# Kernel optimization log

Hardware: AMD Instinct MI355X
Metric: run time of the kernel (lower is better)

The kernel has to match this reference:

```python
import jax, jax.numpy as jnp
import numpy as np

N_AGENTS = 16
NE = 128
ED = 96          # entity_shape (entity_last_action=False)
HE = 128         # hypernet_embed
MD = 32          # mixing_embed_dim
NH = 4           # attn heads
HD = HE // NH
BS, T = 32, 50


def setup_inputs() -> dict:
    key = jax.random.key(0)
    ks = jax.random.split(key, 20)
    def lin(k, i, o):
        return (jax.random.normal(k, (i, o), jnp.float32) / np.sqrt(i)).astype(jnp.float32)
    inp = {
        "agent_qs": jax.random.normal(ks[0], (BS, T, N_AGENTS), jnp.float32),
        "entities": jax.random.normal(ks[1], (BS, T, NE, ED), jnp.float32),
        "entity_mask": jax.random.uniform(ks[2], (BS, T, NE)) < 0.15,  # True = masked/inactive
    }
    for i, p in enumerate(["w1", "v"]):
        b = 3 + i * 6
        inp[p + "_fc1_w"] = lin(ks[b], ED, HE)
        inp[p + "_fc1_b"] = jnp.zeros((HE,), jnp.float32)
        inp[p + "_attn_in_w"] = lin(ks[b + 1], HE, 3 * HE)   # in_trans (no bias)
        inp[p + "_attn_out_w"] = lin(ks[b + 2], HE, HE)
        inp[p + "_attn_out_b"] = jnp.zeros((HE,), jnp.float32)
        inp[p + "_fc2_w"] = lin(ks[b + 3], HE, MD)
        inp[p + "_fc2_b"] = jnp.zeros((MD,), jnp.float32)
    return inp


def _hypernet(x, emask, fc1_w, fc1_b, in_w, out_w, out_b, fc2_w, fc2_b, mode):
    # x: [B, ne, ed], emask: [B, ne] bool (True = masked)
    B = x.shape[0]
    x1 = jax.nn.relu(x @ fc1_w + fc1_b)                         # [B, ne, HE]
    agent_mask = emask[:, :N_AGENTS]                            # [B, na]
    af = agent_mask.astype(x.dtype)
    ef = emask.astype(x.dtype)
    # attn_mask = 1 - (1-agent)(1-entity); 1 => masked pair
    pre = (1.0 - (1.0 - af)[:, :, None] * (1.0 - ef)[:, None, :]) > 0.5  # [B, na, ne]
    qkv = x1 @ in_w                                             # [B, ne, 3*HE]
    q, k, v = jnp.split(qkv, 3, axis=-1)
    q = q[:, :N_AGENTS].reshape(B, N_AGENTS, NH, HD)
    k = k.reshape(B, NE, NH, HD)
    v = v.reshape(B, NE, NH, HD)
    logits = jnp.einsum('bqhd,bkhd->bhqk', q, k) / np.float32(np.sqrt(HD))
    logits = jnp.where(pre[:, None], jnp.float32(-1e9), logits)
    w = jax.nn.softmax(logits, axis=-1)                         # [B, NH, na, ne]
    # rows where every entity is masked: torch softmax gives NaN -> filled with 0
    all_masked = jnp.all(pre, axis=-1)                          # [B, na]
    w = jnp.where(all_masked[:, None, :, None], 0.0, w)
    attn = jnp.einsum('bhqk,bkhd->bqhd', w, v).reshape(B, N_AGENTS, HE)
    out = attn @ out_w + out_b
    out = jnp.where(agent_mask[:, :, None], 0.0, out)           # post_mask fill
    x3 = out @ fc2_w + fc2_b
    x3 = jnp.where(agent_mask[:, :, None], 0.0, x3)             # [B, na, MD]
    if mode == 'alt_vector':
        return x3.mean(axis=2)                                  # [B, na]
    return x3.mean(axis=(1, 2))                                 # [B]  (scalar mode)


def reference(agent_qs, entities, entity_mask,
              w1_fc1_w, w1_fc1_b, w1_attn_in_w, w1_attn_out_w, w1_attn_out_b, w1_fc2_w, w1_fc2_b,
              v_fc1_w, v_fc1_b, v_attn_in_w, v_attn_out_w, v_attn_out_b, v_fc2_w, v_fc2_b):
    bs, max_t, ne, ed = entities.shape
    ents = entities.reshape(bs * max_t, ne, ed)
    emask = entity_mask.reshape(bs * max_t, ne)
    qs = agent_qs.reshape(-1, N_AGENTS)
    w1 = _hypernet(ents, emask, w1_fc1_w, w1_fc1_b, w1_attn_in_w, w1_attn_out_w,
                   w1_attn_out_b, w1_fc2_w, w1_fc2_b, 'alt_vector')   # [B, na]
    w1 = jnp.abs(w1)                                            # softmax_mixing_weights=False
    v = _hypernet(ents, emask, v_fc1_w, v_fc1_b, v_attn_in_w, v_attn_out_w,
                  v_attn_out_b, v_fc2_w, v_fc2_b, 'scalar')     # [B]
    q_tot = (qs * w1).sum(axis=1) + v
    return q_tot.reshape(bs, max_t, 1)
```

## Files before the change

kernel.cpp:

```cpp
#include <hip/hip_runtime.h>
#include <hip/hip_bf16.h>


#define NA 16
#define NEn 128
#define EDm 96
#define ST 136

typedef __attribute__((ext_vector_type(8))) short bf16x8;
typedef __attribute__((ext_vector_type(4))) float f32x4;

#define MFMA(a, b, c) __builtin_amdgcn_mfma_f32_16x16x32_bf16((a), (b), (c), 0, 0, 0)
#define LGKM0() __asm__ volatile("s_waitcnt lgkmcnt(0)" ::: "memory")

#define OFF_W1 0
#define OFF_WQ 12288
#define OFF_WK 28672
#define OFF_WV 45056
#define OFF_WO 61440
#define OFF_W2 77824
#define HYPE 81920
#define WS_FLAG_OFF 327680

__device__ __forceinline__ unsigned short f2bf(float f) {
  unsigned u = __float_as_uint(f);
  u += 0x7fffu + ((u >> 16) & 1u);
  return (unsigned short)(u >> 16);
}

__device__ __forceinline__ unsigned cvt_pk2(float lo, float hi) {
  union { __hip_bfloat162 h2; unsigned u; } cv;
  cv.h2 = __float22bfloat162_rn(float2{lo, hi});
  return cv.u;
}

__device__ __forceinline__ void ctile_store(unsigned short* dst, int row0,
                                            int col, f32x4 v) {
  unsigned x = cvt_pk2(v[0], v[1]);
  unsigned y = cvt_pk2(v[2], v[3]);
  unsigned ox = (unsigned)__shfl_xor((int)x, 1);
  unsigned oy = (unsigned)__shfl_xor((int)y, 1);
  unsigned w0, w1;
  int ra;
  if ((threadIdx.x & 1) == 0) {
    ra = 0;
    w0 = (x & 0xffffu) | (ox << 16);
    w1 = (x >> 16) | (ox & 0xffff0000u);
  } else {
    ra = 2;
    w0 = (oy & 0xffffu) | (y << 16);
    w1 = (oy >> 16) | (y & 0xffff0000u);
  }
  *(unsigned*)(dst + (row0 + ra) * ST + (col & ~1)) = w0;
  *(unsigned*)(dst + (row0 + ra + 1) * ST + (col & ~1)) = w1;
}

__global__ void prep_kernel(const float* __restrict__ w_fc1w,
                            const float* __restrict__ w_inw,
                            const float* __restrict__ w_outw,
                            const float* __restrict__ w_fc2w,
                            const float* __restrict__ v_fc1w,
                            const float* __restrict__ v_inw,
                            const float* __restrict__ v_outw,
                            const float* __restrict__ v_fc2w,
                            const unsigned char* __restrict__ mask,
                            unsigned short* __restrict__ ws,
                            int* __restrict__ flag) {
  if (blockIdx.x == 80) {
    const uint4 v = *(const uint4*)(mask + threadIdx.x * 16);
    const unsigned nz = (v.x | v.y | v.z | v.w) & 0xffffff00u;
    const int any = __syncthreads_or((int)(nz != 0));
    if (threadIdx.x == 0) *flag = (any == 0) ? 1 : 0;
    return;
  }
  const int g = blockIdx.x * 256 + threadIdx.x;
  const int p = (g >= 10240) ? 1 : 0;
  const int i = g - p * 10240;
  const int l = i & 63;
  const int tt = i >> 6;
  const int lhi = l >> 4, lo = l & 15;
  const float* fc1w = p ? v_fc1w : w_fc1w;
  const float* inw = p ? v_inw : w_inw;
  const float* outw = p ? v_outw : w_outw;
  const float* fc2w = p ? v_fc2w : w_fc2w;
  unsigned short* wsp = ws + p * HYPE;

  float v8[8];
  unsigned short* dst;
  if (tt < 24) {
    const int nt = tt / 3, kt = tt - nt * 3;
    const float* src = fc1w + (kt * 32 + lhi * 8) * 128 + nt * 16 + lo;
#pragma unroll
    for (int j = 0; j < 8; ++j) v8[j] = src[j * 128];
    dst = wsp + OFF_W1 + tt * 512 + l * 8;
  } else if (tt < 56) {
    const int t2 = tt - 24;
    const int nt = t2 >> 2, kt = t2 & 3;
    const float* src = inw + (kt * 32 + lhi * 8) * 384 + nt * 16 + lo;
#pragma unroll
    for (int j = 0; j < 8; ++j) v8[j] = src[j * 384] * 0.17677669529663687f;
    dst = wsp + OFF_WQ + t2 * 512 + l * 8;
  } else if (tt < 88) {
    const int t2 = tt - 56;
    const int h = t2 >> 3, nt = t2 & 7;
    const float* src = inw + (nt * 16 + lo) * 384 + 128 + h * 32 + lhi * 8;
#pragma unroll
    for (int j = 0; j < 8; ++j) v8[j] = src[j];
    dst = wsp + OFF_WK + t2 * 512 + l * 8;
  } else if (tt < 120) {
    const int t2 = tt - 88;
    const int kt = t2 & 3, q = t2 >> 2;
    const int h = q >> 1, mt = q & 1;
    const float* src =
        inw + (kt * 32 + lhi * 8) * 384 + 256 + h * 32 + mt * 16 + lo;
#pragma unroll
    for (int j = 0; j < 8; ++j) v8[j] = src[j * 384];
    dst = wsp + OFF_WV + t2 * 512 + l * 8;
  } else if (tt < 152) {
    const int t2 = tt - 120;
    const int nt = t2 >> 2, kt = t2 & 3;
    const float* src = outw + (kt * 32 + lhi * 8) * 128 + nt * 16 + lo;
#pragma unroll
    for (int j = 0; j < 8; ++j) v8[j] = src[j * 128];
    dst = wsp + OFF_WO + t2 * 512 + l * 8;
  } else {
    const int t2 = tt - 152;
    const int nt = t2 >> 2, kt = t2 & 3;
    const float* src = fc2w + (kt * 32 + lhi * 8) * 32 + nt * 16 + lo;
#pragma unroll
    for (int j = 0; j < 8; ++j) v8[j] = src[j * 32];
    dst = wsp + OFF_W2 + t2 * 512 + l * 8;
  }
  bf16x8 o;
#pragma unroll
  for (int j = 0; j < 8; ++j) o[j] = (short)f2bf(v8[j]);
  *(bf16x8*)dst = o;
}

#define SMEM_BYTES 52480

__global__ __launch_bounds__(256, 2) void qmix_mfma(
    const float* __restrict__ agent_qs, const float* __restrict__ entities,
    const unsigned char* __restrict__ emask_g,
    const unsigned short* __restrict__ wsw, const int* __restrict__ mflag,
    const float* __restrict__ w_fc1b, const float* __restrict__ w_outb,
    const float* __restrict__ w_fc2b, const float* __restrict__ v_fc1b,
    const float* __restrict__ v_outb, const float* __restrict__ v_fc2b,
    float* __restrict__ out_g) {
  const int t = threadIdx.x;
  const int wv = t >> 6;
  const int ln = t & 63;
  const int lr = ln & 15;
  const int lq = ln >> 4;
  const int b = blockIdx.x >> 1;
  const int p = blockIdx.x & 1;
  const float* ents = entities + (size_t)b * (NEn * EDm);

  __shared__ __align__(16) unsigned char smem[SMEM_BYTES];
  unsigned short* sx1 = (unsigned short*)smem;
  unsigned short* sSlice = sx1 + 17408;
  unsigned short* sattn = sSlice;
  unsigned short* sout = sSlice + 16 * ST;
  float* sres = (float*)(smem + 52224);
  unsigned char* sm = smem + 52352;
  unsigned short* sS = sSlice + wv * 16 * ST;

  const int is_i32 = *mflag;
  int mv = 1;
  if (t < NEn) {
    if (is_i32)
      mv = (((const int*)emask_g)[(size_t)b * NEn + t] != 0) ? 1 : 0;
    else
      mv = (emask_g[(size_t)b * NEn + t] != 0) ? 1 : 0;
    sm[t] = (unsigned char)mv;
  }
  const int allE = __syncthreads_and(mv);

  const unsigned short* wsb = wsw + (size_t)p * HYPE;
  const float* fc1b = p ? v_fc1b : w_fc1b;
  const float* outb = p ? v_outb : w_outb;
  const float* fc2b = p ? v_fc2b : w_fc2b;

  {
#pragma unroll
    for (int mi = 0; mi < 2; ++mi) {
      const int mt = wv * 2 + mi;
      bf16x8 af[3];
      const float* erow = ents + (mt * 16 + lr) * EDm + lq * 8;
#pragma unroll
      for (int kt = 0; kt < 3; ++kt) {
        float4 u = *(const float4*)(erow + kt * 32);
        float4 w = *(const float4*)(erow + kt * 32 + 4);
        union { unsigned u32[4]; bf16x8 v8; } cv;
        cv.u32[0] = cvt_pk2(u.x, u.y);
        cv.u32[1] = cvt_pk2(u.z, u.w);
        cv.u32[2] = cvt_pk2(w.x, w.y);
        cv.u32[3] = cvt_pk2(w.z, w.w);
        af[kt] = cv.v8;
      }
#pragma unroll
      for (int nt = 0; nt < 8; ++nt) {
        f32x4 acc = {0.f, 0.f, 0.f, 0.f};
        const unsigned short* bp = wsb + OFF_W1 + (nt * 3) * 512 + ln * 8;
#pragma unroll
        for (int kt = 0; kt < 3; ++kt)
          acc = MFMA(af[kt], *(const bf16x8*)(bp + kt * 512), acc);
        const float bias = fc1b[nt * 16 + lr];
        f32x4 r;
        r[0] = fmaxf(acc[0] + bias, 0.f); r[1] = fmaxf(acc[1] + bias, 0.f);
        r[2] = fmaxf(acc[2] + bias, 0.f); r[3] = fmaxf(acc[3] + bias, 0.f);
        ctile_store(sx1, mt * 16 + lq * 4, nt * 16 + lr, r);
      }
    }
  }
  __syncthreads();

  {
    bf16x8 aq[4];
#pragma unroll
    for (int kt = 0; kt < 4; ++kt)
      aq[kt] = *(const bf16x8*)(sx1 + lr * ST + kt * 32 + lq * 8);
#pragma unroll
    for (int ni = 0; ni < 2; ++ni) {
      const int nt = wv * 2 + ni;
      f32x4 acc = {0.f, 0.f, 0.f, 0.f};
      const unsigned short* bp = wsb + OFF_WQ + (nt * 4) * 512 + ln * 8;
#pragma unroll
      for (int kt = 0; kt < 4; ++kt)
        acc = MFMA(aq[kt], *(const bf16x8*)(bp + kt * 512), acc);
      ctile_store(sS, lq * 4, ni * 16 + lr, acc);
    }
  }
  bf16x8 wk[8];
#pragma unroll
  for (int nt = 0; nt < 8; ++nt)
    wk[nt] = *(const bf16x8*)(wsb + OFF_WK + (wv * 8 + nt) * 512 + ln * 8);
  LGKM0();
  const bf16x8 aQ = *(const bf16x8*)(sS + lr * ST + lq * 8);

  {
    f32x4 Cw[8];
#pragma unroll
    for (int nt = 0; nt < 8; ++nt) {
      f32x4 acc = {0.f, 0.f, 0.f, 0.f};
      Cw[nt] = MFMA(aQ, wk[nt], acc);
    }
#pragma unroll
    for (int nt = 0; nt < 8; ++nt)
      ctile_store(sS, lq * 4, nt * 16 + lr, Cw[nt]);
  }
  LGKM0();
  bf16x8 aw[4];
#pragma unroll
  for (int kt = 0; kt < 4; ++kt)
    aw[kt] = *(const bf16x8*)(sS + lr * ST + kt * 32 + lq * 8);

  f32x4 Cl[8];
  __builtin_amdgcn_s_setprio(1);
#pragma unroll
  for (int nt = 0; nt < 8; ++nt) {
    f32x4 acc = {0.f, 0.f, 0.f, 0.f};
#pragma unroll
    for (int kt = 0; kt < 4; ++kt) {
      const bf16x8 bx =
          *(const bf16x8*)(sx1 + (nt * 16 + lr) * ST + kt * 32 + lq * 8);
      acc = MFMA(aw[kt], bx, acc);
    }
    Cl[nt] = acc;
  }
  __builtin_amdgcn_s_setprio(0);

  {
    float lv[8][4];
#pragma unroll
    for (int nt = 0; nt < 8; ++nt) {
      const int eM = sm[nt * 16 + lr];
#pragma unroll
      for (int r = 0; r < 4; ++r) lv[nt][r] = eM ? -1e9f : Cl[nt][r];
    }
    float mx[4], sl[4];
#pragma unroll
    for (int r = 0; r < 4; ++r) {
      float m = lv[0][r];
#pragma unroll
      for (int nt = 1; nt < 8; ++nt) m = fmaxf(m, lv[nt][r]);
      mx[r] = m;
    }
#pragma unroll
    for (int k = 1; k < 16; k <<= 1)
#pragma unroll
      for (int r = 0; r < 4; ++r) mx[r] = fmaxf(mx[r], __shfl_xor(mx[r], k));
    float ex[8][4];
#pragma unroll
    for (int r = 0; r < 4; ++r) sl[r] = 0.f;
#pragma unroll
    for (int nt = 0; nt < 8; ++nt)
#pragma unroll
      for (int r = 0; r < 4; ++r) {
        ex[nt][r] = __expf(lv[nt][r] - mx[r]);
        sl[r] += ex[nt][r];
      }
#pragma unroll
    for (int k = 1; k < 16; k <<= 1)
#pragma unroll
      for (int r = 0; r < 4; ++r) sl[r] += __shfl_xor(sl[r], k);
    float sc[4];
#pragma unroll
    for (int r = 0; r < 4; ++r)
      sc[r] = ((int)sm[lq * 4 + r] | allE) ? 0.f : (1.f / sl[r]);
#pragma unroll
    for (int nt = 0; nt < 8; ++nt) {
      f32x4 wv4;
#pragma unroll
      for (int r = 0; r < 4; ++r) wv4[r] = ex[nt][r] * sc[r];
      ctile_store(sS, lq * 4, nt * 16 + lr, wv4);
    }
  }
  LGKM0();
  bf16x8 aw2[4];
#pragma unroll
  for (int kt = 0; kt < 4; ++kt)
    aw2[kt] = *(const bf16x8*)(sS + lr * ST + kt * 32 + lq * 8);

  f32x4 Cv[2][8];
  __builtin_amdgcn_s_setprio(1);
#pragma unroll
  for (int mt = 0; mt < 2; ++mt) {
    bf16x8 av[4];
#pragma unroll
    for (int kt = 0; kt < 4; ++kt)
      av[kt] = *(const bf16x8*)(wsb + OFF_WV +
                                (((wv * 2 + mt) * 4) + kt) * 512 + ln * 8);
#pragma unroll
    for (int nt = 0; nt < 8; ++nt) {
      f32x4 acc = {0.f, 0.f, 0.f, 0.f};
#pragma unroll
      for (int kt = 0; kt < 4; ++kt) {
        const bf16x8 bx =
            *(const bf16x8*)(sx1 + (nt * 16 + lr) * ST + kt * 32 + lq * 8);
        acc = MFMA(av[kt], bx, acc);
      }
      Cv[mt][nt] = acc;
    }
  }
  __builtin_amdgcn_s_setprio(0);
  __syncthreads();

  {
#pragma unroll
    for (int mt = 0; mt < 2; ++mt)
#pragma unroll
      for (int nt = 0; nt < 8; ++nt)
        ctile_store(sx1, wv * 32 + mt * 16 + lq * 4, nt * 16 + lr,
                    Cv[mt][nt]);
  }
  LGKM0();
  {
#pragma unroll
    for (int ntd = 0; ntd < 2; ++ntd) {
      f32x4 acc = {0.f, 0.f, 0.f, 0.f};
#pragma unroll
      for (int kt = 0; kt < 4; ++kt) {
        const bf16x8 bv = *(const bf16x8*)(sx1 + (wv * 32 + ntd * 16 + lr) *
                                                     ST +
                                           kt * 32 + lq * 8);
        acc = MFMA(aw2[kt], bv, acc);
      }
      ctile_store(sattn, lq * 4, wv * 32 + ntd * 16 + lr, acc);
    }
  }
  bf16x8 wo[2][4];
#pragma unroll
  for (int ni = 0; ni < 2; ++ni) {
    const unsigned short* bp =
        wsb + OFF_WO + ((wv * 2 + ni) * 4) * 512 + ln * 8;
#pragma unroll
    for (int kt = 0; kt < 4; ++kt)
      wo[ni][kt] = *(const bf16x8*)(bp + kt * 512);
  }
  __syncthreads();

  {
    bf16x8 aa[4];
#pragma unroll
    for (int kt = 0; kt < 4; ++kt)
      aa[kt] = *(const bf16x8*)(sattn + lr * ST + kt * 32 + lq * 8);
#pragma unroll
    for (int ni = 0; ni < 2; ++ni) {
      const int nt = wv * 2 + ni;
      f32x4 acc = {0.f, 0.f, 0.f, 0.f};
#pragma unroll
      for (int kt = 0; kt < 4; ++kt)
        acc = MFMA(aa[kt], wo[ni][kt], acc);
      const float bj = outb[nt * 16 + lr];
      f32x4 r;
      r[0] = acc[0] + bj; r[1] = acc[1] + bj;
      r[2] = acc[2] + bj; r[3] = acc[3] + bj;
      ctile_store(sout, lq * 4, nt * 16 + lr, r);
    }
  }
  bf16x8 w2f[2][4];
#pragma unroll
  for (int nt = 0; nt < 2; ++nt) {
    const unsigned short* bp = wsb + OFF_W2 + (nt * 4) * 512 + ln * 8;
#pragma unroll
    for (int kt = 0; kt < 4; ++kt)
      w2f[nt][kt] = *(const bf16x8*)(bp + kt * 512);
  }
  __syncthreads();

  {
    bf16x8 ao[4];
#pragma unroll
    for (int kt = 0; kt < 4; ++kt)
      ao[kt] = *(const bf16x8*)(sout + lr * ST + kt * 32 + lq * 8);
    f32x4 Cx[2];
#pragma unroll
    for (int nt = 0; nt < 2; ++nt) {
      f32x4 acc = {0.f, 0.f, 0.f, 0.f};
#pragma unroll
      for (int kt = 0; kt < 4; ++kt)
        acc = MFMA(ao[kt], w2f[nt][kt], acc);
      Cx[nt] = acc;
    }
    const float b0 = fc2b[lr], b1 = fc2b[16 + lr];
    float rs[4];
#pragma unroll
    for (int r = 0; r < 4; ++r) {
      const int row = lq * 4 + r;
      rs[r] = sm[row] ? 0.f : (Cx[0][r] + b0 + Cx[1][r] + b1);
    }
#pragma unroll
    for (int k = 1; k < 16; k <<= 1)
#pragma unroll
      for (int r = 0; r < 4; ++r) rs[r] += __shfl_xor(rs[r], k);
    if (wv == 0 && lr == 0) {
#pragma unroll
      for (int r = 0; r < 4; ++r) {
        const int q = lq * 4 + r;
        sres[q] = p ? rs[r] : fabsf(rs[r]) * (1.f / 32.f);
      }
    }
  }

  __syncthreads();
  if (t == 0) {
    float s = 0.f;
    if (p == 0) {
      const float* qs = agent_qs + (size_t)b * NA;
#pragma unroll
      for (int q = 0; q < NA; ++q) s += qs[q] * sres[q];
    } else {
#pragma unroll
      for (int q = 0; q < NA; ++q) s += sres[q];
      s *= (1.f / 512.f);
    }
    atomicAdd(out_g + b, s);
  }
}

extern "C" void kernel_launch(void* const* d_in, const int* in_sizes, int n_in,
                              void* d_out, int out_size, void* d_ws,
                              size_t ws_size, hipStream_t stream) {
  (void)n_in; (void)out_size; (void)ws_size;
  const int nb = in_sizes[0] / NA;
  unsigned short* wsw = (unsigned short*)d_ws;
  int* mflag = (int*)((char*)d_ws + WS_FLAG_OFF);

  hipLaunchKernelGGL(prep_kernel, dim3(81), dim3(256), 0, stream,
                     (const float*)d_in[3], (const float*)d_in[5],
                     (const float*)d_in[6], (const float*)d_in[8],
                     (const float*)d_in[10], (const float*)d_in[12],
                     (const float*)d_in[13], (const float*)d_in[15],
                     (const unsigned char*)d_in[2], wsw, mflag);
  hipLaunchKernelGGL(qmix_mfma, dim3(nb * 2), dim3(256), 0, stream,
                     (const float*)d_in[0], (const float*)d_in[1],
                     (const unsigned char*)d_in[2], (const unsigned short*)wsw,
                     (const int*)mflag, (const float*)d_in[4],
                     (const float*)d_in[7], (const float*)d_in[9],
                     (const float*)d_in[11], (const float*)d_in[14],
                     (const float*)d_in[16], (float*)d_out);
}
```

Baseline: 253.0 us.

## Interleave softmax between V-projection halves and hoist entity loads

Splits the V-projection MFMA loop into two halves and places the softmax VALU work between them, so exponentials and shuffles can overlap with matrix-core work. Entity-row global loads are moved to the start of the kernel, before the mask load and block barrier, to hide their latency. The final block barrier is replaced with an LDS wait, since the result row is written and read within wave 0. The cost is more live registers (staged entity values, Cl, Cv0 and the softmax arrays), which may raise VGPR use and lower occupancy.

Result: faster. 243.7 us (-3.7%).

```diff
diff --git a/kernel.cpp b/kernel.cpp
--- a/kernel.cpp
+++ b/kernel.cpp
@@ -165,6 +165,17 @@
   unsigned char* sm = smem + 52352;
   unsigned short* sS = sSlice + wv * 16 * ST;
 
+  float4 eu[2][3], ev[2][3];
+#pragma unroll
+  for (int mi = 0; mi < 2; ++mi) {
+    const float* erow = ents + ((wv * 2 + mi) * 16 + lr) * EDm + lq * 8;
+#pragma unroll
+    for (int kt = 0; kt < 3; ++kt) {
+      eu[mi][kt] = *(const float4*)(erow + kt * 32);
+      ev[mi][kt] = *(const float4*)(erow + kt * 32 + 4);
+    }
+  }
+
   const int is_i32 = *mflag;
   int mv = 1;
   if (t < NEn) {
@@ -186,16 +197,13 @@
     for (int mi = 0; mi < 2; ++mi) {
       const int mt = wv * 2 + mi;
       bf16x8 af[3];
-      const float* erow = ents + (mt * 16 + lr) * EDm + lq * 8;
 #pragma unroll
       for (int kt = 0; kt < 3; ++kt) {
-        float4 u = *(const float4*)(erow + kt * 32);
-        float4 w = *(const float4*)(erow + kt * 32 + 4);
         union { unsigned u32[4]; bf16x8 v8; } cv;
-        cv.u32[0] = cvt_pk2(u.x, u.y);
-        cv.u32[1] = cvt_pk2(u.z, u.w);
-        cv.u32[2] = cvt_pk2(w.x, w.y);
-        cv.u32[3] = cvt_pk2(w.z, w.w);
+        cv.u32[0] = cvt_pk2(eu[mi][kt].x, eu[mi][kt].y);
+        cv.u32[1] = cvt_pk2(eu[mi][kt].z, eu[mi][kt].w);
+        cv.u32[2] = cvt_pk2(ev[mi][kt].x, ev[mi][kt].y);
+        cv.u32[3] = cvt_pk2(ev[mi][kt].z, ev[mi][kt].w);
         af[kt] = cv.v8;
       }
 #pragma unroll
@@ -268,69 +276,14 @@
     }
     Cl[nt] = acc;
   }
-  __builtin_amdgcn_s_setprio(0);
-
-  {
-    float lv[8][4];
-#pragma unroll
-    for (int nt = 0; nt < 8; ++nt) {
-      const int eM = sm[nt * 16 + lr];
-#pragma unroll
-      for (int r = 0; r < 4; ++r) lv[nt][r] = eM ? -1e9f : Cl[nt][r];
-    }
-    float mx[4], sl[4];
-#pragma unroll
-    for (int r = 0; r < 4; ++r) {
-      float m = lv[0][r];
-#pragma unroll
-      for (int nt = 1; nt < 8; ++nt) m = fmaxf(m, lv[nt][r]);
-      mx[r] = m;
-    }
-#pragma unroll
-    for (int k = 1; k < 16; k <<= 1)
-#pragma unroll
-      for (int r = 0; r < 4; ++r) mx[r] = fmaxf(mx[r], __shfl_xor(mx[r], k));
-    float ex[8][4];
-#pragma unroll
-    for (int r = 0; r < 4; ++r) sl[r] = 0.f;
-#pragma unroll
-    for (int nt = 0; nt < 8; ++nt)
-#pragma unroll
-      for (int r = 0; r < 4; ++r) {
-        ex[nt][r] = __expf(lv[nt][r] - mx[r]);
-        sl[r] += ex[nt][r];
-      }
-#pragma unroll
-    for (int k = 1; k < 16; k <<= 1)
-#pragma unroll
-      for (int r = 0; r < 4; ++r) sl[r] += __shfl_xor(sl[r], k);
-    float sc[4];
-#pragma unroll
-    for (int r = 0; r < 4; ++r)
-      sc[r] = ((int)sm[lq * 4 + r] | allE) ? 0.f : (1.f / sl[r]);
-#pragma unroll
-    for (int nt = 0; nt < 8; ++nt) {
-      f32x4 wv4;
-#pragma unroll
-      for (int r = 0; r < 4; ++r) wv4[r] = ex[nt][r] * sc[r];
-      ctile_store(sS, lq * 4, nt * 16 + lr, wv4);
-    }
-  }
-  LGKM0();
-  bf16x8 aw2[4];
-#pragma unroll
-  for (int kt = 0; kt < 4; ++kt)
-    aw2[kt] = *(const bf16x8*)(sS + lr * ST + kt * 32 + lq * 8);
-
-  f32x4 Cv[2][8];
-  __builtin_amdgcn_s_setprio(1);
-#pragma unroll
-  for (int mt = 0; mt < 2; ++mt) {
+
+  f32x4 Cv0[8], Cv1[8];
+  {
     bf16x8 av[4];
 #pragma unroll
     for (int kt = 0; kt < 4; ++kt)
-      av[kt] = *(const bf16x8*)(wsb + OFF_WV +
-                                (((wv * 2 + mt) * 4) + kt) * 512 + ln * 8);
+      av[kt] = *(const bf16x8*)(wsb + OFF_WV + ((wv * 2) * 4 + kt) * 512 +
+                                ln * 8);
 #pragma unroll
     for (int nt = 0; nt < 8; ++nt) {
       f32x4 acc = {0.f, 0.f, 0.f, 0.f};
@@ -340,19 +293,92 @@
             *(const bf16x8*)(sx1 + (nt * 16 + lr) * ST + kt * 32 + lq * 8);
         acc = MFMA(av[kt], bx, acc);
       }
-      Cv[mt][nt] = acc;
+      Cv0[nt] = acc;
     }
   }
   __builtin_amdgcn_s_setprio(0);
+
+  {
+    float lv[8][4];
+#pragma unroll
+    for (int nt = 0; nt < 8; ++nt) {
+      const int eM = sm[nt * 16 + lr];
+#pragma unroll
+      for (int r = 0; r < 4; ++r) lv[nt][r] = eM ? -1e9f : Cl[nt][r];
+    }
+    float mx[4], sl[4];
+#pragma unroll
+    for (int r = 0; r < 4; ++r) {
+      float m = lv[0][r];
+#pragma unroll
+      for (int nt = 1; nt < 8; ++nt) m = fmaxf(m, lv[nt][r]);
+      mx[r] = m;
+    }
+#pragma unroll
+    for (int k = 1; k < 16; k <<= 1)
+#pragma unroll
+      for (int r = 0; r < 4; ++r) mx[r] = fmaxf(mx[r], __shfl_xor(mx[r], k));
+    float ex[8][4];
+#pragma unroll
+    for (int r = 0; r < 4; ++r) sl[r] = 0.f;
+#pragma unroll
+    for (int nt = 0; nt < 8; ++nt)
+#pragma unroll
+      for (int r = 0; r < 4; ++r) {
+        ex[nt][r] = __expf(lv[nt][r] - mx[r]);
+        sl[r] += ex[nt][r];
+      }
+#pragma unroll
+    for (int k = 1; k < 16; k <<= 1)
+#pragma unroll
+      for (int r = 0; r < 4; ++r) sl[r] += __shfl_xor(sl[r], k);
+    float sc[4];
+#pragma unroll
+    for (int r = 0; r < 4; ++r)
+      sc[r] = ((int)sm[lq * 4 + r] | allE) ? 0.f : (1.f / sl[r]);
+#pragma unroll
+    for (int nt = 0; nt < 8; ++nt) {
+      f32x4 wv4;
+#pragma unroll
+      for (int r = 0; r < 4; ++r) wv4[r] = ex[nt][r] * sc[r];
+      ctile_store(sS, lq * 4, nt * 16 + lr, wv4);
+    }
+  }
+
+  __builtin_amdgcn_s_setprio(1);
+  {
+    bf16x8 av[4];
+#pragma unroll
+    for (int kt = 0; kt < 4; ++kt)
+      av[kt] = *(const bf16x8*)(wsb + OFF_WV + ((wv * 2 + 1) * 4 + kt) * 512 +
+                                ln * 8);
+#pragma unroll
+    for (int nt = 0; nt < 8; ++nt) {
+      f32x4 acc = {0.f, 0.f, 0.f, 0.f};
+#pragma unroll
+      for (int kt = 0; kt < 4; ++kt) {
+        const bf16x8 bx =
+            *(const bf16x8*)(sx1 + (nt * 16 + lr) * ST + kt * 32 + lq * 8);
+        acc = MFMA(av[kt], bx, acc);
+      }
+      Cv1[nt] = acc;
+    }
+  }
+  __builtin_amdgcn_s_setprio(0);
+  LGKM0();
+  bf16x8 aw2[4];
+#pragma unroll
+  for (int kt = 0; kt < 4; ++kt)
+    aw2[kt] = *(const bf16x8*)(sS + lr * ST + kt * 32 + lq * 8);
   __syncthreads();
 
   {
 #pragma unroll
-    for (int mt = 0; mt < 2; ++mt)
-#pragma unroll
-      for (int nt = 0; nt < 8; ++nt)
-        ctile_store(sx1, wv * 32 + mt * 16 + lq * 4, nt * 16 + lr,
-                    Cv[mt][nt]);
+    for (int nt = 0; nt < 8; ++nt)
+      ctile_store(sx1, wv * 32 + lq * 4, nt * 16 + lr, Cv0[nt]);
+#pragma unroll
+    for (int nt = 0; nt < 8; ++nt)
+      ctile_store(sx1, wv * 32 + 16 + lq * 4, nt * 16 + lr, Cv1[nt]);
   }
   LGKM0();
   {
@@ -443,7 +469,7 @@
     }
   }
 
-  __syncthreads();
+  LGKM0();
   if (t == 0) {
     float s = 0.f;
     if (p == 0) {
```
